# Kernel tuning notes

Hardware: AMD Instinct MI355X
Metric: run time of the kernel (lower is better)

The kernel has to match this reference:

```python
import jax, jax.numpy as jnp
import numpy as np

N = 100_000   # nodes
E = 1_600_000 # edges
F = 16        # input node features
H = 32        # embedding_size
B = 256       # graphs in batch


def setup_inputs() -> dict:
    key = jax.random.key(0)
    ks = jax.random.split(key, 13)
    s = 0.1  # small init scale for weights
    return {
        "x": jax.random.normal(ks[0], (N, F), jnp.float32),
        "edge_index": jax.random.randint(ks[1], (2, E), 0, N, dtype=jnp.int64),
        "batch_index": jnp.sort(jax.random.randint(ks[2], (N,), 0, B, dtype=jnp.int64)),
        "W0": jax.random.normal(ks[3], (F, H), jnp.float32) * s,
        "b0": jax.random.normal(ks[4], (H,), jnp.float32) * s,
        "W1": jax.random.normal(ks[5], (H, H), jnp.float32) * s,
        "b1": jax.random.normal(ks[6], (H,), jnp.float32) * s,
        "W2": jax.random.normal(ks[7], (H, H), jnp.float32) * s,
        "b2": jax.random.normal(ks[8], (H,), jnp.float32) * s,
        "W3": jax.random.normal(ks[9], (H, H), jnp.float32) * s,
        "b3": jax.random.normal(ks[10], (H, H), jnp.float32)[:, 0] * s,
        "W_out": jax.random.normal(ks[11], (3 * H, 1), jnp.float32) * s,
        "b_out": jax.random.normal(ks[12], (1,), jnp.float32) * s,
    }


def _gcn_forward(x, edge_index, batch_index,
                 W0, b0, W1, b1, W2, b2, W3, b3, W_out, b_out):
    src, dst = edge_index[0], edge_index[1]
    n = x.shape[0]
    # GCN symmetric normalization with self-loops: deg includes the +1 self-loop
    deg = jax.ops.segment_sum(jnp.ones(src.shape[0], x.dtype), dst, num_segments=n) + 1.0
    dinv = jax.lax.rsqrt(deg)
    edge_coef = (dinv[src] * dinv[dst])[:, None]   # [E,1]
    self_coef = (dinv * dinv)[:, None]             # [N,1]

    def conv(h, W, b):
        # x' = D^{-1/2}(A+I)D^{-1/2} (h W) + b  (PyG GCNConv)
        hW = h @ W
        agg = jax.ops.segment_sum(hW[src] * edge_coef, dst, num_segments=n)
        agg = agg + hW * self_coef  # self-loop contribution
        return agg + b

    h = jnp.tanh(conv(x, W0, b0))
    h = jnp.tanh(conv(h, W1, b1))
    h = jnp.tanh(conv(h, W2, b2))
    h = jnp.tanh(conv(h, W3, b3))

    # Global max / mean / add pooling over batch_index
    gmax = jax.ops.segment_max(h, batch_index, num_segments=B)
    gsum = jax.ops.segment_sum(h, batch_index, num_segments=B)
    cnt = jax.ops.segment_sum(jnp.ones(n, h.dtype), batch_index, num_segments=B)
    gmean = gsum / jnp.maximum(cnt, 1.0)[:, None]
    pooled = jnp.concatenate([gmax, gmean, gsum], axis=1)  # [B, 3H]

    out = pooled @ W_out + b_out  # [B, 1]
    return out, pooled


def reference(x, edge_index, batch_index,
              W0, b0, W1, b1, W2, b2, W3, b3, W_out, b_out):
    return _gcn_forward(x, edge_index, batch_index,
                        W0, b0, W1, b1, W2, b2, W3, b3, W_out, b_out)
```

## Files before the change

### kernel.cpp

```cpp
#include <hip/hip_runtime.h>
#include <math.h>

#define N_NODES 100000
#define N_EDGES 1600000
#define F_IN    16
#define H_DIM   32
#define B_GRAPHS 256

#define BSHIFT  7
#define BSIZE   128
#define NBUCKET ((N_NODES + BSIZE - 1) / BSIZE)
#define EPB     8192
#define NCHUNK  ((N_EDGES + EPB - 1) / EPB)
#define CAPB    2560
#define CSTRIDE 2944
#define TPAD    (NBUCKET * CSTRIDE)
#define CURSTR  16
#define NPB     16
#define LAYER_BLOCKS (N_NODES / NPB)

__device__ inline float bf_lo(unsigned u) { return __uint_as_float(u << 16); }
__device__ inline float bf_hi(unsigned u) { return __uint_as_float(u & 0xffff0000u); }
__device__ inline unsigned pack_bf16x2(float a, float b) {
    unsigned ua = __float_as_uint(a), ub = __float_as_uint(b);
    ua += 0x7fffu + ((ua >> 16) & 1u);
    ub += 0x7fffu + ((ub >> 16) & 1u);
    return (ua >> 16) | (ub & 0xffff0000u);
}

__global__ __launch_bounds__(256) void init_cur_kernel(int* __restrict__ bucket_cur) {
    int b = blockIdx.x * 256 + threadIdx.x;
    if (b < NBUCKET) bucket_cur[b * CURSTR] = b * CAPB;
}

__global__ __launch_bounds__(1024) void passB_kernel(const int* __restrict__ ei,
                                                     int* __restrict__ bucket_cur,
                                                     unsigned* __restrict__ rec_out) {
    __shared__ int hist[NBUCKET];
    __shared__ int gcur[NBUCKET];
    int t = threadIdx.x;
    for (int k = t; k < NBUCKET; k += 1024) hist[k] = 0;
    __syncthreads();

    const int* dst = ei + N_EDGES;
    int base = blockIdx.x * EPB;
    int end  = base + EPB; if (end > N_EDGES) end = N_EDGES;

    for (int e = base + t; e < end; e += 1024) atomicAdd(&hist[dst[e] >> BSHIFT], 1);
    __syncthreads();

    for (int k = t; k < NBUCKET; k += 1024) {
        int h = hist[k];
        gcur[k] = h ? atomicAdd(&bucket_cur[k * CURSTR], h) : 0;
    }
    __syncthreads();

    for (int e = base + t; e < end; e += 1024) {
        int d = dst[e], s = ei[e];
        int bk = d >> BSHIFT;
        int pos = atomicAdd(&gcur[bk], 1);
        rec_out[pos] = (unsigned)s | ((unsigned)(d & (BSIZE - 1)) << 20);
    }
}

__global__ __launch_bounds__(256) void dinv_kernel(const unsigned* __restrict__ rec,
                                                   const int* __restrict__ bucket_cur,
                                                   float* __restrict__ dinv) {
    __shared__ int cnt[BSIZE];
    int t = threadIdx.x, b = blockIdx.x;
    if (t < BSIZE) cnt[t] = 0;
    __syncthreads();
    int e1 = bucket_cur[b * CURSTR];
    for (int e = b * CAPB + t; e < e1; e += 256) atomicAdd(&cnt[rec[e] >> 20], 1);
    __syncthreads();
    int nd = (b << BSHIFT) + t;
    if (t < BSIZE && nd < N_NODES) dinv[nd] = rsqrtf((float)cnt[t] + 1.0f);
}

__global__ __launch_bounds__(256) void passC_kernel(const unsigned* __restrict__ rec,
                                                    const int* __restrict__ bucket_cur,
                                                    const float* __restrict__ dinv,
                                                    int2* __restrict__ row_meta,
                                                    int2* __restrict__ csr) {
    __shared__ unsigned stage[CAPB];
    __shared__ int cnt[BSIZE];
    __shared__ int pds[BSIZE];
    __shared__ int cur[BSIZE];
    __shared__ float sdv[BSIZE];
    int t = threadIdx.x, b = blockIdx.x;
    int node0 = b << BSHIFT;
    int e0 = b * CAPB;
    int n = bucket_cur[b * CURSTR] - e0;
    int pbase = b * CSTRIDE;
    if (t < BSIZE) {
        cnt[t] = 0;
        int nd = node0 + t;
        sdv[t] = (nd < N_NODES) ? dinv[nd] : 0.f;
    }
    __syncthreads();
    for (int k = t; k < n; k += 256) {
        unsigned r = rec[e0 + k];
        stage[k] = r;
        atomicAdd(&cnt[r >> 20], 1);
    }
    __syncthreads();
    int pd = 0;
    if (t < BSIZE) { pd = (cnt[t] + 3) & ~3; pds[t] = pd; }
    __syncthreads();
    for (int off = 1; off < BSIZE; off <<= 1) {
        int v = (t < BSIZE && t >= off) ? pds[t - off] : 0;
        __syncthreads();
        if (t < BSIZE) pds[t] += v;
        __syncthreads();
    }
    if (t < BSIZE) {
        int startp = pbase + pds[t] - pd;
        cur[t] = startp;
        int nd = node0 + t;
        if (nd < N_NODES) {
            row_meta[nd] = make_int2(startp, pd);
            for (int k = startp + cnt[t]; k < startp + pd; ++k)
                csr[k] = make_int2(nd, 0);
        }
    }
    __syncthreads();
    for (int k = t; k < n; k += 256) {
        unsigned r = stage[k];
        int dl = r >> 20;
        int s  = r & 0xFFFFF;
        int pos = atomicAdd(&cur[dl], 1);
        csr[pos] = make_int2(s, __float_as_int(dinv[s] * sdv[dl]));
    }
}

template <int FIN, bool PACKED>
__global__ __launch_bounds__(256) void layer_kernel(
        const void* __restrict__ h_in_v,
        const int2* __restrict__ row_meta,
        const int4* __restrict__ csr4,
        const float* __restrict__ dinv,
        const float* __restrict__ W,
        const float* __restrict__ bias,
        unsigned* __restrict__ h_out) {
    constexpr int STR = FIN + 1;
    __shared__ float sW[FIN * H_DIM];
    __shared__ float sb[H_DIM];
    __shared__ float agg[NPB][STR];
    int t = threadIdx.x;
    for (int k = t; k < FIN * H_DIM; k += 256) sW[k] = W[k];
    if (t < H_DIM) sb[t] = bias[t];

    int nl = t >> 4, ln = t & 15;
    int i = blockIdx.x * NPB + nl;
    int2 m = row_meta[i];
    float di = dinv[i], di2 = di * di;
    int q    = m.x >> 1;
    int qend = (m.x + m.y) >> 1;

    if (PACKED) {
        const unsigned* hp = (const unsigned*)h_in_v;
        unsigned u = hp[i * 16 + ln];
        float acc0 = bf_lo(u) * di2, acc1 = bf_hi(u) * di2;
        for (; q + 8 <= qend; q += 8) {
            int4 ca[8];
#pragma unroll
            for (int k = 0; k < 8; ++k) ca[k] = csr4[q + k];
            unsigned v[16];
#pragma unroll
            for (int k = 0; k < 8; ++k) {
                v[2 * k]     = hp[ca[k].x * 16 + ln];
                v[2 * k + 1] = hp[ca[k].z * 16 + ln];
            }
#pragma unroll
            for (int k = 0; k < 8; ++k) {
                float c0 = __int_as_float(ca[k].y), c1 = __int_as_float(ca[k].w);
                acc0 += bf_lo(v[2 * k]) * c0 + bf_lo(v[2 * k + 1]) * c1;
                acc1 += bf_hi(v[2 * k]) * c0 + bf_hi(v[2 * k + 1]) * c1;
            }
        }
        if (q + 4 <= qend) {
            int4 ca[4];
#pragma unroll
            for (int k = 0; k < 4; ++k) ca[k] = csr4[q + k];
#pragma unroll
            for (int k = 0; k < 4; ++k) {
                unsigned v0 = hp[ca[k].x * 16 + ln], v1 = hp[ca[k].z * 16 + ln];
                float c0 = __int_as_float(ca[k].y), c1 = __int_as_float(ca[k].w);
                acc0 += bf_lo(v0) * c0 + bf_lo(v1) * c1;
                acc1 += bf_hi(v0) * c0 + bf_hi(v1) * c1;
            }
            q += 4;
        }
        if (q < qend) {
            int4 a = csr4[q], b = csr4[q + 1];
            unsigned v0 = hp[a.x * 16 + ln], v1 = hp[a.z * 16 + ln];
            unsigned v2 = hp[b.x * 16 + ln], v3 = hp[b.z * 16 + ln];
            float c0 = __int_as_float(a.y), c1 = __int_as_float(a.w);
            float c2 = __int_as_float(b.y), c3 = __int_as_float(b.w);
            acc0 += bf_lo(v0) * c0 + bf_lo(v1) * c1 + bf_lo(v2) * c2 + bf_lo(v3) * c3;
            acc1 += bf_hi(v0) * c0 + bf_hi(v1) * c1 + bf_hi(v2) * c2 + bf_hi(v3) * c3;
        }
        agg[nl][2 * ln]     = acc0;
        agg[nl][2 * ln + 1] = acc1;
    } else {
        const float* xf = (const float*)h_in_v;
        float acc = xf[i * F_IN + ln] * di2;
        for (; q + 8 <= qend; q += 8) {
            int4 ca[8];
#pragma unroll
            for (int k = 0; k < 8; ++k) ca[k] = csr4[q + k];
            float v[16];
#pragma unroll
            for (int k = 0; k < 8; ++k) {
                v[2 * k]     = xf[ca[k].x * F_IN + ln];
                v[2 * k + 1] = xf[ca[k].z * F_IN + ln];
            }
#pragma unroll
            for (int k = 0; k < 8; ++k)
                acc += v[2 * k] * __int_as_float(ca[k].y)
                     + v[2 * k + 1] * __int_as_float(ca[k].w);
        }
        if (q + 4 <= qend) {
            int4 ca[4];
#pragma unroll
            for (int k = 0; k < 4; ++k) ca[k] = csr4[q + k];
#pragma unroll
            for (int k = 0; k < 4; ++k)
                acc += xf[ca[k].x * F_IN + ln] * __int_as_float(ca[k].y)
                     + xf[ca[k].z * F_IN + ln] * __int_as_float(ca[k].w);
            q += 4;
        }
        if (q < qend) {
            int4 a = csr4[q], b = csr4[q + 1];
            acc += xf[a.x * F_IN + ln] * __int_as_float(a.y)
                 + xf[a.z * F_IN + ln] * __int_as_float(a.w)
                 + xf[b.x * F_IN + ln] * __int_as_float(b.y)
                 + xf[b.z * F_IN + ln] * __int_as_float(b.w);
        }
        agg[nl][ln] = acc;
    }
    __syncthreads();

    int j0 = 2 * ln;
    float o0 = sb[j0], o1 = sb[j0 + 1];
    const float* arow = &agg[nl][0];
#pragma unroll
    for (int k = 0; k < FIN; ++k) {
        float a = arow[k];
        o0 += a * sW[k * H_DIM + j0];
        o1 += a * sW[k * H_DIM + j0 + 1];
    }
    h_out[i * 16 + ln] = pack_bf16x2(tanhf(o0), tanhf(o1));
}

__global__ __launch_bounds__(256) void pool_kernel(const unsigned* __restrict__ hp,
                                                   const int* __restrict__ batch,
                                                   const float* __restrict__ Wout,
                                                   const float* __restrict__ bout,
                                                   float* __restrict__ out) {
    int b = blockIdx.x;
    int t = threadIdx.x;
    int lane_n = t >> 5;
    int j = t & 31;

    int lo = 0, hi = N_NODES;
    while (lo < hi) { int mid = (lo + hi) >> 1; if (batch[mid] < b) lo = mid + 1; else hi = mid; }
    int start = lo;
    hi = N_NODES;
    while (lo < hi) { int mid = (lo + hi) >> 1; if (batch[mid] < b + 1) lo = mid + 1; else hi = mid; }
    int end = lo;

    float vmax = -INFINITY, vsum = 0.f;
    for (int i = start + lane_n; i < end; i += 8) {
        unsigned q = hp[i * 16 + (j >> 1)];
        float v = (j & 1) ? bf_hi(q) : bf_lo(q);
        vmax = fmaxf(vmax, v);
        vsum += v;
    }

    __shared__ float smax[8][32];
    __shared__ float ssum[8][32];
    __shared__ float pool96[96];
    smax[lane_n][j] = vmax;
    ssum[lane_n][j] = vsum;
    __syncthreads();

    if (t < 32) {
        float m = smax[0][t], s = ssum[0][t];
#pragma unroll
        for (int n = 1; n < 8; ++n) { m = fmaxf(m, smax[n][t]); s += ssum[n][t]; }
        int cnt = end - start;
        float mean = s / fmaxf((float)cnt, 1.0f);
        pool96[t]      = m;
        pool96[32 + t] = mean;
        pool96[64 + t] = s;
    }
    __syncthreads();

    if (t < 96) out[B_GRAPHS + b * 96 + t] = pool96[t];

    __shared__ float dotbuf[96];
    if (t < 96) dotbuf[t] = pool96[t] * Wout[t];
    __syncthreads();
    if (t == 0) {
        float acc = 0.f;
#pragma unroll
        for (int k = 0; k < 96; ++k) acc += dotbuf[k];
        out[b] = acc + bout[0];
    }
}

extern "C" void kernel_launch(void* const* d_in, const int* in_sizes, int n_in,
                              void* d_out, int out_size, void* d_ws, size_t ws_size,
                              hipStream_t stream) {
    const float* x     = (const float*)d_in[0];
    const int*   ei    = (const int*)  d_in[1];
    const int*   batch = (const int*)  d_in[2];
    const float* W0    = (const float*)d_in[3];
    const float* b0    = (const float*)d_in[4];
    const float* W1    = (const float*)d_in[5];
    const float* b1    = (const float*)d_in[6];
    const float* W2    = (const float*)d_in[7];
    const float* b2    = (const float*)d_in[8];
    const float* W3    = (const float*)d_in[9];
    const float* b3    = (const float*)d_in[10];
    const float* Wout  = (const float*)d_in[11];
    const float* bout  = (const float*)d_in[12];
    float* out = (float*)d_out;

    char* p = (char*)d_ws;
    float*    dinv       = (float*)p;    p += (size_t)N_NODES * 4;
    unsigned* hA         = (unsigned*)p; p += (size_t)N_NODES * 16 * 4;
    unsigned* rec        = (unsigned*)p; p += (size_t)NBUCKET * CAPB * 4;
    int2*     csr        = (int2*)p;     p += (size_t)TPAD * 8;
    int2*     row_meta   = (int2*)p;     p += (size_t)N_NODES * 8;
    int*      bucket_cur = (int*)p;      p += (size_t)NBUCKET * CURSTR * 4;
    unsigned* hB = rec;

    init_cur_kernel<<<(NBUCKET + 255) / 256, 256, 0, stream>>>(bucket_cur);
    passB_kernel<<<NCHUNK, 1024, 0, stream>>>(ei, bucket_cur, rec);
    dinv_kernel<<<NBUCKET, 256, 0, stream>>>(rec, bucket_cur, dinv);
    passC_kernel<<<NBUCKET, 256, 0, stream>>>(rec, bucket_cur, dinv, row_meta, csr);

    layer_kernel<F_IN, false><<<LAYER_BLOCKS, 256, 0, stream>>>(
        x,  row_meta, (const int4*)csr, dinv, W0, b0, hA);
    layer_kernel<H_DIM, true><<<LAYER_BLOCKS, 256, 0, stream>>>(
        hA, row_meta, (const int4*)csr, dinv, W1, b1, hB);
    layer_kernel<H_DIM, true><<<LAYER_BLOCKS, 256, 0, stream>>>(
        hB, row_meta, (const int4*)csr, dinv, W2, b2, hA);
    layer_kernel<H_DIM, true><<<LAYER_BLOCKS, 256, 0, stream>>>(
        hA, row_meta, (const int4*)csr, dinv, W3, b3, hB);

    pool_kernel<<<B_GRAPHS, 256, 0, stream>>>(hB, batch, Wout, bout, out);
}
```

Baseline: 259.5 us.

## Split each node's edge list across two thread groups and shrink passB chunks

Each node's neighbor list is now split in half between two 16-lane groups. The two partial sums are combined in shared memory before the dense transform, which now uses one thread per output column and a shuffle to pack bf16 pairs. The goal is to double memory-level parallelism per node and shorten the per-row gather critical path, at the cost of twice as many blocks and some extra shared-memory traffic. The edge bucketing pass also uses smaller chunks with 512-thread blocks, which gives more blocks but more global atomics on the bucket cursors.

```diff
diff --git a/kernel.cpp b/kernel.cpp
--- a/kernel.cpp
+++ b/kernel.cpp
@@ -10,13 +10,13 @@
 #define BSHIFT  7
 #define BSIZE   128
 #define NBUCKET ((N_NODES + BSIZE - 1) / BSIZE)
-#define EPB     8192
+#define EPB     4096
 #define NCHUNK  ((N_EDGES + EPB - 1) / EPB)
 #define CAPB    2560
 #define CSTRIDE 2944
 #define TPAD    (NBUCKET * CSTRIDE)
 #define CURSTR  16
-#define NPB     16
+#define NPB     8
 #define LAYER_BLOCKS (N_NODES / NPB)
 
 __device__ inline float bf_lo(unsigned u) { return __uint_as_float(u << 16); }
@@ -33,29 +33,29 @@
     if (b < NBUCKET) bucket_cur[b * CURSTR] = b * CAPB;
 }
 
-__global__ __launch_bounds__(1024) void passB_kernel(const int* __restrict__ ei,
-                                                     int* __restrict__ bucket_cur,
-                                                     unsigned* __restrict__ rec_out) {
+__global__ __launch_bounds__(512) void passB_kernel(const int* __restrict__ ei,
+                                                    int* __restrict__ bucket_cur,
+                                                    unsigned* __restrict__ rec_out) {
     __shared__ int hist[NBUCKET];
     __shared__ int gcur[NBUCKET];
     int t = threadIdx.x;
-    for (int k = t; k < NBUCKET; k += 1024) hist[k] = 0;
+    for (int k = t; k < NBUCKET; k += 512) hist[k] = 0;
     __syncthreads();
 
     const int* dst = ei + N_EDGES;
     int base = blockIdx.x * EPB;
     int end  = base + EPB; if (end > N_EDGES) end = N_EDGES;
 
-    for (int e = base + t; e < end; e += 1024) atomicAdd(&hist[dst[e] >> BSHIFT], 1);
-    __syncthreads();
-
-    for (int k = t; k < NBUCKET; k += 1024) {
+    for (int e = base + t; e < end; e += 512) atomicAdd(&hist[dst[e] >> BSHIFT], 1);
+    __syncthreads();
+
+    for (int k = t; k < NBUCKET; k += 512) {
         int h = hist[k];
         gcur[k] = h ? atomicAdd(&bucket_cur[k * CURSTR], h) : 0;
     }
     __syncthreads();
 
-    for (int e = base + t; e < end; e += 1024) {
+    for (int e = base + t; e < end; e += 512) {
         int d = dst[e], s = ei[e];
         int bk = d >> BSHIFT;
         int pos = atomicAdd(&gcur[bk], 1);
@@ -145,22 +145,32 @@
     constexpr int STR = FIN + 1;
     __shared__ float sW[FIN * H_DIM];
     __shared__ float sb[H_DIM];
-    __shared__ float agg[NPB][STR];
+    __shared__ float agg[2][NPB][STR];
     int t = threadIdx.x;
     for (int k = t; k < FIN * H_DIM; k += 256) sW[k] = W[k];
     if (t < H_DIM) sb[t] = bias[t];
 
-    int nl = t >> 4, ln = t & 15;
+    int grp = t >> 4;
+    int nl  = grp >> 1;
+    int g   = grp & 1;
+    int ln  = t & 15;
     int i = blockIdx.x * NPB + nl;
     int2 m = row_meta[i];
     float di = dinv[i], di2 = di * di;
-    int q    = m.x >> 1;
-    int qend = (m.x + m.y) >> 1;
+    int half = ((m.y >> 1) + 3) & ~3;
+    int h0   = half < m.y ? half : m.y;
+    int s0   = m.x + (g ? h0 : 0);
+    int s1   = g ? (m.x + m.y) : (m.x + h0);
+    int q    = s0 >> 1;
+    int qend = s1 >> 1;
 
     if (PACKED) {
         const unsigned* hp = (const unsigned*)h_in_v;
-        unsigned u = hp[i * 16 + ln];
-        float acc0 = bf_lo(u) * di2, acc1 = bf_hi(u) * di2;
+        float acc0 = 0.f, acc1 = 0.f;
+        if (g == 0) {
+            unsigned u = hp[i * 16 + ln];
+            acc0 = bf_lo(u) * di2; acc1 = bf_hi(u) * di2;
+        }
         for (; q + 8 <= qend; q += 8) {
             int4 ca[8];
 #pragma unroll
@@ -200,11 +210,11 @@
             acc0 += bf_lo(v0) * c0 + bf_lo(v1) * c1 + bf_lo(v2) * c2 + bf_lo(v3) * c3;
             acc1 += bf_hi(v0) * c0 + bf_hi(v1) * c1 + bf_hi(v2) * c2 + bf_hi(v3) * c3;
         }
-        agg[nl][2 * ln]     = acc0;
-        agg[nl][2 * ln + 1] = acc1;
+        agg[g][nl][2 * ln]     = acc0;
+        agg[g][nl][2 * ln + 1] = acc1;
     } else {
         const float* xf = (const float*)h_in_v;
-        float acc = xf[i * F_IN + ln] * di2;
+        float acc = (g == 0) ? xf[i * F_IN + ln] * di2 : 0.f;
         for (; q + 8 <= qend; q += 8) {
             int4 ca[8];
 #pragma unroll
@@ -237,20 +247,19 @@
                  + xf[b.x * F_IN + ln] * __int_as_float(b.y)
                  + xf[b.z * F_IN + ln] * __int_as_float(b.w);
         }
-        agg[nl][ln] = acc;
-    }
-    __syncthreads();
-
-    int j0 = 2 * ln;
-    float o0 = sb[j0], o1 = sb[j0 + 1];
-    const float* arow = &agg[nl][0];
-#pragma unroll
-    for (int k = 0; k < FIN; ++k) {
-        float a = arow[k];
-        o0 += a * sW[k * H_DIM + j0];
-        o1 += a * sW[k * H_DIM + j0 + 1];
-    }
-    h_out[i * 16 + ln] = pack_bf16x2(tanhf(o0), tanhf(o1));
+        agg[g][nl][ln] = acc;
+    }
+    __syncthreads();
+
+    int nl2 = t >> 5, j = t & 31;
+    int i2 = blockIdx.x * NPB + nl2;
+    float o = sb[j];
+#pragma unroll
+    for (int k = 0; k < FIN; ++k)
+        o += (agg[0][nl2][k] + agg[1][nl2][k]) * sW[k * H_DIM + j];
+    o = tanhf(o);
+    float o_pair = __shfl_xor(o, 1);
+    if (!(j & 1)) h_out[i2 * 16 + (j >> 1)] = pack_bf16x2(o, o_pair);
 }
 
 __global__ __launch_bounds__(256) void pool_kernel(const unsigned* __restrict__ hp,
@@ -338,7 +347,7 @@
     unsigned* hB = rec;
 
     init_cur_kernel<<<(NBUCKET + 255) / 256, 256, 0, stream>>>(bucket_cur);
-    passB_kernel<<<NCHUNK, 1024, 0, stream>>>(ei, bucket_cur, rec);
+    passB_kernel<<<NCHUNK, 512, 0, stream>>>(ei, bucket_cur, rec);
     dinv_kernel<<<NBUCKET, 256, 0, stream>>>(rec, bucket_cur, dinv);
     passC_kernel<<<NBUCKET, 256, 0, stream>>>(rec, bucket_cur, dinv, row_meta, csr);
 
```

Result: slower. 303.9 us (+17.1%).

## Store intermediate GCN activations in custom 8-bit float and stream CSR nontemporally

Applied to the files above, without the earlier changes.

Intermediate node embeddings between layers are now stored as a custom 8-bit float with 4 exponent and 3 mantissa bits, exponent-shifted by 2^-120, instead of bf16. This halves the bytes per neighbour gather in the sparse aggregation. The final layer still writes bf16 for pooling. CSR edge records are read with nontemporal loads so they do not pollute the cache used by the gathers. The cost is a large loss of precision in the hidden activations, which may exceed tolerance, plus extra decode ALU work per gathered value.

```diff
diff --git a/kernel.cpp b/kernel.cpp
--- a/kernel.cpp
+++ b/kernel.cpp
@@ -19,6 +19,8 @@
 #define NPB     16
 #define LAYER_BLOCKS (N_NODES / NPB)
 
+typedef int v4i __attribute__((ext_vector_type(4)));
+
 __device__ inline float bf_lo(unsigned u) { return __uint_as_float(u << 16); }
 __device__ inline float bf_hi(unsigned u) { return __uint_as_float(u & 0xffff0000u); }
 __device__ inline unsigned pack_bf16x2(float a, float b) {
@@ -26,6 +28,21 @@
     ua += 0x7fffu + ((ua >> 16) & 1u);
     ub += 0x7fffu + ((ub >> 16) & 1u);
     return (ua >> 16) | (ub & 0xffff0000u);
+}
+
+__device__ inline unsigned f32_to_fp8(float v) {
+    unsigned u = __float_as_uint(v * 0x1.0p-120f);
+    unsigned s = (u >> 24) & 0x80u;
+    u &= 0x7FFFFFFFu;
+    u += 0x7FFFFu + ((u >> 20) & 1u);
+    unsigned em = u >> 20;
+    if (em > 0x7Eu) em = 0x7Eu;
+    return s | em;
+}
+__device__ inline float fp8_to_f32(unsigned b) {
+    unsigned s  = (b & 0x80u) << 24;
+    unsigned em = (b & 0x7Fu) << 20;
+    return __uint_as_float(s | em) * 0x1.0p120f;
 }
 
 __global__ __launch_bounds__(256) void init_cur_kernel(int* __restrict__ bucket_cur) {
@@ -137,11 +154,12 @@
 __global__ __launch_bounds__(256) void layer_kernel(
         const void* __restrict__ h_in_v,
         const int2* __restrict__ row_meta,
-        const int4* __restrict__ csr4,
+        const v4i* __restrict__ csr4,
         const float* __restrict__ dinv,
         const float* __restrict__ W,
         const float* __restrict__ bias,
-        unsigned* __restrict__ h_out) {
+        unsigned short* __restrict__ out8,
+        unsigned* __restrict__ outbf) {
     constexpr int STR = FIN + 1;
     __shared__ float sW[FIN * H_DIM];
     __shared__ float sb[H_DIM];
@@ -158,13 +176,14 @@
     int qend = (m.x + m.y) >> 1;
 
     if (PACKED) {
-        const unsigned* hp = (const unsigned*)h_in_v;
-        unsigned u = hp[i * 16 + ln];
-        float acc0 = bf_lo(u) * di2, acc1 = bf_hi(u) * di2;
+        const unsigned short* hp = (const unsigned short*)h_in_v;
+        unsigned su = hp[i * 16 + ln];
+        float acc0 = fp8_to_f32(su & 0xFF) * di2;
+        float acc1 = fp8_to_f32(su >> 8) * di2;
         for (; q + 8 <= qend; q += 8) {
-            int4 ca[8];
-#pragma unroll
-            for (int k = 0; k < 8; ++k) ca[k] = csr4[q + k];
+            v4i ca[8];
+#pragma unroll
+            for (int k = 0; k < 8; ++k) ca[k] = __builtin_nontemporal_load(&csr4[q + k]);
             unsigned v[16];
 #pragma unroll
             for (int k = 0; k < 8; ++k) {
@@ -174,31 +193,35 @@
 #pragma unroll
             for (int k = 0; k < 8; ++k) {
                 float c0 = __int_as_float(ca[k].y), c1 = __int_as_float(ca[k].w);
-                acc0 += bf_lo(v[2 * k]) * c0 + bf_lo(v[2 * k + 1]) * c1;
-                acc1 += bf_hi(v[2 * k]) * c0 + bf_hi(v[2 * k + 1]) * c1;
+                unsigned u0 = v[2 * k], u1 = v[2 * k + 1];
+                acc0 += fp8_to_f32(u0 & 0xFF) * c0 + fp8_to_f32(u1 & 0xFF) * c1;
+                acc1 += fp8_to_f32(u0 >> 8)   * c0 + fp8_to_f32(u1 >> 8)   * c1;
             }
         }
         if (q + 4 <= qend) {
-            int4 ca[4];
-#pragma unroll
-            for (int k = 0; k < 4; ++k) ca[k] = csr4[q + k];
+            v4i ca[4];
+#pragma unroll
+            for (int k = 0; k < 4; ++k) ca[k] = __builtin_nontemporal_load(&csr4[q + k]);
 #pragma unroll
             for (int k = 0; k < 4; ++k) {
-                unsigned v0 = hp[ca[k].x * 16 + ln], v1 = hp[ca[k].z * 16 + ln];
+                unsigned u0 = hp[ca[k].x * 16 + ln], u1 = hp[ca[k].z * 16 + ln];
                 float c0 = __int_as_float(ca[k].y), c1 = __int_as_float(ca[k].w);
-                acc0 += bf_lo(v0) * c0 + bf_lo(v1) * c1;
-                acc1 += bf_hi(v0) * c0 + bf_hi(v1) * c1;
+                acc0 += fp8_to_f32(u0 & 0xFF) * c0 + fp8_to_f32(u1 & 0xFF) * c1;
+                acc1 += fp8_to_f32(u0 >> 8)   * c0 + fp8_to_f32(u1 >> 8)   * c1;
             }
             q += 4;
         }
         if (q < qend) {
-            int4 a = csr4[q], b = csr4[q + 1];
-            unsigned v0 = hp[a.x * 16 + ln], v1 = hp[a.z * 16 + ln];
-            unsigned v2 = hp[b.x * 16 + ln], v3 = hp[b.z * 16 + ln];
+            v4i a = __builtin_nontemporal_load(&csr4[q]);
+            v4i b = __builtin_nontemporal_load(&csr4[q + 1]);
+            unsigned u0 = hp[a.x * 16 + ln], u1 = hp[a.z * 16 + ln];
+            unsigned u2 = hp[b.x * 16 + ln], u3 = hp[b.z * 16 + ln];
             float c0 = __int_as_float(a.y), c1 = __int_as_float(a.w);
             float c2 = __int_as_float(b.y), c3 = __int_as_float(b.w);
-            acc0 += bf_lo(v0) * c0 + bf_lo(v1) * c1 + bf_lo(v2) * c2 + bf_lo(v3) * c3;
-            acc1 += bf_hi(v0) * c0 + bf_hi(v1) * c1 + bf_hi(v2) * c2 + bf_hi(v3) * c3;
+            acc0 += fp8_to_f32(u0 & 0xFF) * c0 + fp8_to_f32(u1 & 0xFF) * c1
+                  + fp8_to_f32(u2 & 0xFF) * c2 + fp8_to_f32(u3 & 0xFF) * c3;
+            acc1 += fp8_to_f32(u0 >> 8) * c0 + fp8_to_f32(u1 >> 8) * c1
+                  + fp8_to_f32(u2 >> 8) * c2 + fp8_to_f32(u3 >> 8) * c3;
         }
         agg[nl][2 * ln]     = acc0;
         agg[nl][2 * ln + 1] = acc1;
@@ -206,9 +229,9 @@
         const float* xf = (const float*)h_in_v;
         float acc = xf[i * F_IN + ln] * di2;
         for (; q + 8 <= qend; q += 8) {
-            int4 ca[8];
-#pragma unroll
-            for (int k = 0; k < 8; ++k) ca[k] = csr4[q + k];
+            v4i ca[8];
+#pragma unroll
+            for (int k = 0; k < 8; ++k) ca[k] = __builtin_nontemporal_load(&csr4[q + k]);
             float v[16];
 #pragma unroll
             for (int k = 0; k < 8; ++k) {
@@ -221,9 +244,9 @@
                      + v[2 * k + 1] * __int_as_float(ca[k].w);
         }
         if (q + 4 <= qend) {
-            int4 ca[4];
-#pragma unroll
-            for (int k = 0; k < 4; ++k) ca[k] = csr4[q + k];
+            v4i ca[4];
+#pragma unroll
+            for (int k = 0; k < 4; ++k) ca[k] = __builtin_nontemporal_load(&csr4[q + k]);
 #pragma unroll
             for (int k = 0; k < 4; ++k)
                 acc += xf[ca[k].x * F_IN + ln] * __int_as_float(ca[k].y)
@@ -231,7 +254,8 @@
             q += 4;
         }
         if (q < qend) {
-            int4 a = csr4[q], b = csr4[q + 1];
+            v4i a = __builtin_nontemporal_load(&csr4[q]);
+            v4i b = __builtin_nontemporal_load(&csr4[q + 1]);
             acc += xf[a.x * F_IN + ln] * __int_as_float(a.y)
                  + xf[a.z * F_IN + ln] * __int_as_float(a.w)
                  + xf[b.x * F_IN + ln] * __int_as_float(b.y)
@@ -250,7 +274,9 @@
         o0 += a * sW[k * H_DIM + j0];
         o1 += a * sW[k * H_DIM + j0 + 1];
     }
-    h_out[i * 16 + ln] = pack_bf16x2(tanhf(o0), tanhf(o1));
+    o0 = tanhf(o0); o1 = tanhf(o1);
+    if (out8)  out8[i * 16 + ln]  = (unsigned short)(f32_to_fp8(o0) | (f32_to_fp8(o1) << 8));
+    if (outbf) outbf[i * 16 + ln] = pack_bf16x2(o0, o1);
 }
 
 __global__ __launch_bounds__(256) void pool_kernel(const unsigned* __restrict__ hp,
@@ -329,13 +355,14 @@
     float* out = (float*)d_out;
 
     char* p = (char*)d_ws;
-    float*    dinv       = (float*)p;    p += (size_t)N_NODES * 4;
-    unsigned* hA         = (unsigned*)p; p += (size_t)N_NODES * 16 * 4;
-    unsigned* rec        = (unsigned*)p; p += (size_t)NBUCKET * CAPB * 4;
-    int2*     csr        = (int2*)p;     p += (size_t)TPAD * 8;
-    int2*     row_meta   = (int2*)p;     p += (size_t)N_NODES * 8;
-    int*      bucket_cur = (int*)p;      p += (size_t)NBUCKET * CURSTR * 4;
-    unsigned* hB = rec;
+    float*          dinv       = (float*)p;          p += (size_t)N_NODES * 4;
+    unsigned short* h8A        = (unsigned short*)p; p += (size_t)N_NODES * 16 * 2;
+    unsigned short* h8B        = (unsigned short*)p; p += (size_t)N_NODES * 16 * 2;
+    unsigned*       rec        = (unsigned*)p;       p += (size_t)NBUCKET * CAPB * 4;
+    int2*           csr        = (int2*)p;           p += (size_t)TPAD * 8;
+    int2*           row_meta   = (int2*)p;           p += (size_t)N_NODES * 8;
+    int*            bucket_cur = (int*)p;            p += (size_t)NBUCKET * CURSTR * 4;
+    unsigned* hBF = rec;
 
     init_cur_kernel<<<(NBUCKET + 255) / 256, 256, 0, stream>>>(bucket_cur);
     passB_kernel<<<NCHUNK, 1024, 0, stream>>>(ei, bucket_cur, rec);
@@ -343,13 +370,13 @@
     passC_kernel<<<NBUCKET, 256, 0, stream>>>(rec, bucket_cur, dinv, row_meta, csr);
 
     layer_kernel<F_IN, false><<<LAYER_BLOCKS, 256, 0, stream>>>(
-        x,  row_meta, (const int4*)csr, dinv, W0, b0, hA);
+        x,   row_meta, (const v4i*)csr, dinv, W0, b0, h8A, (unsigned*)nullptr);
     layer_kernel<H_DIM, true><<<LAYER_BLOCKS, 256, 0, stream>>>(
-        hA, row_meta, (const int4*)csr, dinv, W1, b1, hB);
+        h8A, row_meta, (const v4i*)csr, dinv, W1, b1, h8B, (unsigned*)nullptr);
     layer_kernel<H_DIM, true><<<LAYER_BLOCKS, 256, 0, stream>>>(
-        hB, row_meta, (const int4*)csr, dinv, W2, b2, hA);
+        h8B, row_meta, (const v4i*)csr, dinv, W2, b2, h8A, (unsigned*)nullptr);
     layer_kernel<H_DIM, true><<<LAYER_BLOCKS, 256, 0, stream>>>(
-        hA, row_meta, (const int4*)csr, dinv, W3, b3, hB);
-
-    pool_kernel<<<B_GRAPHS, 256, 0, stream>>>(hB, batch, Wout, bout, out);
-}
+        h8A, row_meta, (const v4i*)csr, dinv, W3, b3, (unsigned short*)nullptr, hBF);
+
+    pool_kernel<<<B_GRAPHS, 256, 0, stream>>>(hBF, batch, Wout, bout, out);
+}
```

After: 319.8 us. 1.23x slower.
